# Performance work log

Measured on AMD Instinct MI355X. Metric: run time of the kernel, lower is better.

Reference implementation:

```python
import jax, jax.numpy as jnp
import numpy as np

NX, NY = 512, 512
NT = 240
STRIDE = 4
H = 1e-3
DT = 5e-8
F0 = 100000.0
T0 = 6e-6
AMP = 1.0
GAUSS_A = 5e6
RHO = 1600.0
C_INIT = dict(C11=1e11, C22=1e10, C12=8e9, C16=2.5e10, C26=3e9, C66=1.2e10)
C_LO, C_HI = 1e9, 1e13


def setup_inputs() -> dict:
    # Ricker wavelet source signal (full time resolution)
    t = np.arange(NT) * DT
    tau = t - T0
    pf = (np.pi * F0 * tau) ** 2
    signal = (AMP * (1.0 - 2.0 * pf) * np.exp(-pf)).astype(np.float32)
    # Gaussian point-load spatial distribution centered at (0,0)
    Lx, Ly = H * (NX - 1), H * (NY - 1)
    x = np.linspace(-Lx / 2, Lx / 2, NX, dtype=np.float64)
    y = np.linspace(-Ly / 2, Ly / 2, NY, dtype=np.float64)
    X, Y = np.meshgrid(x, y, indexing='ij')
    r2 = X ** 2 + Y ** 2
    gauss = (GAUSS_A / np.pi * np.exp(-GAUSS_A * r2)).astype(np.float32)
    return {
        'log_C11': jnp.array([np.log(C_INIT['C11'])], dtype=jnp.float32),
        'log_C22': jnp.array([np.log(C_INIT['C22'])], dtype=jnp.float32),
        'log_C12': jnp.array([np.log(C_INIT['C12'])], dtype=jnp.float32),
        'log_C16': jnp.array([np.log(C_INIT['C16'])], dtype=jnp.float32),
        'log_C26': jnp.array([np.log(C_INIT['C26'])], dtype=jnp.float32),
        'log_C66': jnp.array([np.log(C_INIT['C66'])], dtype=jnp.float32),
        'rho': jnp.array([RHO], dtype=jnp.float32),
        'source_signal': jnp.asarray(signal),
        'gaussian_dist': jnp.asarray(gauss),
    }


def _stencils(u, h_inv_sq):
    # u: (B, nx, ny), zero-padded 3x3 FD stencils (conv2d_fixed equivalent)
    p = jnp.pad(u, ((0, 0), (1, 1), (1, 1)))
    dxx = (p[:, 2:, 1:-1] + p[:, :-2, 1:-1] - 2.0 * u) * h_inv_sq
    dyy = (p[:, 1:-1, 2:] + p[:, 1:-1, :-2] - 2.0 * u) * h_inv_sq
    dxy = 0.25 * (p[:, :-2, :-2] - p[:, :-2, 2:] - p[:, 2:, :-2] + p[:, 2:, 2:]) * h_inv_sq
    return dxx, dyy, dxy


def _simulate(log_Cs, rho, source_signal, gaussian_dist):
    log_C11, log_C22, log_C12, log_C16, log_C26, log_C66 = log_Cs
    C11 = jnp.clip(jnp.exp(log_C11[0]), C_LO, C_HI)
    C22 = jnp.clip(jnp.exp(log_C22[0]), C_LO, C_HI)
    C12 = jnp.clip(jnp.exp(log_C12[0]), C_LO, C_HI)
    C16 = jnp.clip(jnp.exp(log_C16[0]), C_LO, C_HI)
    C26 = jnp.clip(jnp.exp(log_C26[0]), C_LO, C_HI)
    C66 = jnp.clip(jnp.exp(log_C66[0]), C_LO, C_HI)
    r = rho[0]
    h_inv_sq = jnp.float32(1.0 / (H * H))
    dt2 = jnp.float32(DT * DT)
    g = gaussian_dist[None]  # (1, nx, ny)
    zeros = jnp.zeros((1, NX, NY), dtype=jnp.float32)

    def step(carry, f_amp):
        ux1, uy1, ux2, uy2 = carry
        # source on y component
        force_y = f_amp * g
        dxx_ux, dyy_ux, dxy_ux = _stencils(ux1, h_inv_sq)
        dxx_uy, dyy_uy, dxy_uy = _stencils(uy1, h_inv_sq)
        Lux = (C11 * dxx_ux + C66 * dyy_ux + (C12 + C66) * dxy_uy
               + 2.0 * C16 * dxy_ux + C16 * dxx_uy + C26 * dyy_uy) / r
        Luy = (C66 * dxx_uy + C22 * dyy_uy + (C12 + C66) * dxy_ux
               + C16 * dxx_ux + C26 * dyy_ux + 2.0 * C26 * dxy_uy + force_y) / r
        ux_new = 2.0 * ux1 - ux2 + dt2 * Lux
        uy_new = 2.0 * uy1 - uy2 + dt2 * Luy
        return (ux_new, uy_new, ux1, uy1), (ux_new, uy_new)

    init = (zeros, zeros, zeros, zeros)
    _, (ux_hist, uy_hist) = jax.lax.scan(step, init, source_signal)
    # (nt, 1, nx, ny) -> (1, nt, nx, ny), then PRIMARY time stride subsample
    ux_fields = jnp.moveaxis(ux_hist, 0, 1)[:, ::STRIDE]
    uy_fields = jnp.moveaxis(uy_hist, 0, 1)[:, ::STRIDE]
    return ux_fields, uy_fields


def reference(log_C11, log_C22, log_C12, log_C16, log_C26, log_C66, rho, source_signal, gaussian_dist):
    return _simulate((log_C11, log_C22, log_C12, log_C16, log_C26, log_C66),
                     rho, source_signal, gaussian_dist)
```

## Files before the change

kernel.cpp:

```cpp
#include <hip/hip_runtime.h>

#define NXg    512
#define Sg     262144
#define NFRg   60
#define Kg     8
#define NCHUNK 30
#define TIg    32
#define TJg    16
#define EIg    48
#define EJg    32
#define RCIg   46
#define RCJg   30
#define CELg   (RCIg*RCJg)
#define NTHRg  512
#define NSLOTg 3

__global__ __launch_bounds__(NTHRg)
void cfrp_init(float* __restrict__ ws)
{
    const int gt = (int)blockIdx.x * NTHRg + (int)threadIdx.x;
    ((float4*)ws)[gt] = make_float4(0.f, 0.f, 0.f, 0.f);
}

__global__ __launch_bounds__(NTHRg, 4)
void cfrp_chunk(const float* __restrict__ lc11, const float* __restrict__ lc22,
                const float* __restrict__ lc12, const float* __restrict__ lc16,
                const float* __restrict__ lc26, const float* __restrict__ lc66,
                const float* __restrict__ rho_p, const float* __restrict__ sig,
                const float* __restrict__ gauss, float* __restrict__ out,
                const float* __restrict__ gcx, const float* __restrict__ gcy,
                const float* __restrict__ gpx, const float* __restrict__ gpy,
                float* __restrict__ ncx, float* __restrict__ ncy,
                float* __restrict__ npx, float* __restrict__ npy,
                int T0)
{
    __shared__ float sf[2][EIg * EJg * 2];

    const int tid = (int)threadIdx.x;
    const int bi = (int)blockIdx.x >> 5;
    const int bj = (int)blockIdx.x & 31;
    const int oi = bi * TIg - Kg;
    const int oj = bj * TJg - Kg;

    const float C11 = fminf(fmaxf(expf(lc11[0]), 1e9f), 1e13f);
    const float C22 = fminf(fmaxf(expf(lc22[0]), 1e9f), 1e13f);
    const float C12 = fminf(fmaxf(expf(lc12[0]), 1e9f), 1e13f);
    const float C16 = fminf(fmaxf(expf(lc16[0]), 1e9f), 1e13f);
    const float C26 = fminf(fmaxf(expf(lc26[0]), 1e9f), 1e13f);
    const float C66 = fminf(fmaxf(expf(lc66[0]), 1e9f), 1e13f);
    const float r    = rho_p[0];
    const float dt2  = 2.5e-15f;
    const float kk   = dt2 * 1e6f / r;
    const float kc11 = kk * C11, kc22 = kk * C22, kc66 = kk * C66;
    const float kc16 = kk * C16, kc26 = kk * C26;
    const float kc1266 = kk * (C12 + C66);
    const float kc16x2 = 2.0f * kc16;
    const float kc26x2 = 2.0f * kc26;
    const float gsc = dt2 / r;

    #pragma unroll
    for (int s = 0; s < NSLOTg; ++s) {
        const int idx = tid + s * NTHRg;
        const int rr = idx >> 5;
        const int cc = idx & 31;
        const int gi = oi + rr, gj = oj + cc;
        const bool inbb = ((unsigned)gi < NXg) && ((unsigned)gj < NXg);
        const int go = gi * NXg + gj;
        const float vx = inbb ? gcx[go] : 0.0f;
        const float vy = inbb ? gcy[go] : 0.0f;
        sf[0][2 * idx]     = vx;  sf[0][2 * idx + 1] = vy;
        sf[1][2 * idx]     = vx;  sf[1][2 * idx + 1] = vy;
    }

    int   la[NSLOTg], go[NSLOTg];
    float pvx[NSLOTg], pvy[NSLOTg], cvx[NSLOTg], cvy[NSLOTg], gfv[NSLOTg];
    bool  act[NSLOTg], inb[NSLOTg], own[NSLOTg];
    #pragma unroll
    for (int s = 0; s < NSLOTg; ++s) {
        const int idx = tid + s * NTHRg;
        act[s] = idx < CELg;
        const int ii = act[s] ? idx : 0;
        const int rr = ii / RCJg + 1;
        const int cc = ii - (rr - 1) * RCJg + 1;
        la[s] = ((rr << 5) + cc) * 2;
        const int gi = oi + rr, gj = oj + cc;
        inb[s] = ((unsigned)gi < NXg) && ((unsigned)gj < NXg);
        go[s] = gi * NXg + gj;
        own[s] = act[s] && rr >= Kg && rr < Kg + TIg
                        && cc >= Kg && cc < Kg + TJg;
        const bool ld = act[s] && inb[s];
        pvx[s] = ld ? gpx[go[s]] : 0.0f;
        pvy[s] = ld ? gpy[go[s]] : 0.0f;
        gfv[s] = ld ? gauss[go[s]] * gsc : 0.0f;
    }
    __syncthreads();

    #pragma unroll
    for (int s = 0; s < NSLOTg; ++s) {
        cvx[s] = sf[0][la[s]];
        cvy[s] = sf[0][la[s] + 1];
    }

    const float* cur = sf[0];
    float*       nxt = sf[1];

    #pragma unroll
    for (int st = 0; st < Kg; ++st) {
        const float fa = sig[T0 + st];
        #pragma unroll
        for (int s = 0; s < NSLOTg; ++s) {
            const int a = la[s];
            const float2 Nn = *(const float2*)&cur[a - 2 * EJg];
            const float2 Ss = *(const float2*)&cur[a + 2 * EJg];
            const float2 Ww = *(const float2*)&cur[a - 2];
            const float2 Ee = *(const float2*)&cur[a + 2];
            const float2 NW = *(const float2*)&cur[a - 2 * EJg - 2];
            const float2 NE = *(const float2*)&cur[a - 2 * EJg + 2];
            const float2 SW = *(const float2*)&cur[a + 2 * EJg - 2];
            const float2 SE = *(const float2*)&cur[a + 2 * EJg + 2];
            const float cx = cvx[s], cy = cvy[s];

            const float sxx_x = Nn.x + Ss.x - 2.0f * cx;
            const float syy_x = Ww.x + Ee.x - 2.0f * cx;
            const float sxy_x = 0.25f * (NW.x - NE.x - SW.x + SE.x);
            const float sxx_y = Nn.y + Ss.y - 2.0f * cy;
            const float syy_y = Ww.y + Ee.y - 2.0f * cy;
            const float sxy_y = 0.25f * (NW.y - NE.y - SW.y + SE.y);

            const float lux = kc11 * sxx_x + kc66 * syy_x + kc1266 * sxy_y
                            + kc16x2 * sxy_x + kc16 * sxx_y + kc26 * syy_y;
            const float luy = kc66 * sxx_y + kc22 * syy_y + kc1266 * sxy_x
                            + kc16 * sxx_x + kc26 * syy_x + kc26x2 * sxy_y
                            + fa * gfv[s];

            float vx = 2.0f * cx - pvx[s] + lux;
            float vy = 2.0f * cy - pvy[s] + luy;
            vx = inb[s] ? vx : 0.0f;
            vy = inb[s] ? vy : 0.0f;
            pvx[s] = cx;  pvy[s] = cy;
            cvx[s] = vx;  cvy[s] = vy;

            if (act[s]) {
                nxt[a]     = vx;
                nxt[a + 1] = vy;
            }
            if ((st & 3) == 0) {
                if (own[s]) {
                    const int fo = ((T0 + st) >> 2) * Sg + go[s];
                    out[fo] = vx;
                    out[fo + NFRg * Sg] = vy;
                }
            }
        }
        __syncthreads();
        float* tmp = (float*)cur; cur = nxt; nxt = tmp;
    }

    #pragma unroll
    for (int s = 0; s < NSLOTg; ++s) {
        if (own[s]) {
            ncx[go[s]] = cvx[s];
            ncy[go[s]] = cvy[s];
            npx[go[s]] = pvx[s];
            npy[go[s]] = pvy[s];
        }
    }
}

extern "C" void kernel_launch(void* const* d_in, const int* in_sizes, int n_in,
                              void* d_out, int out_size, void* d_ws, size_t ws_size,
                              hipStream_t stream) {
    const float* lc11  = (const float*)d_in[0];
    const float* lc22  = (const float*)d_in[1];
    const float* lc12  = (const float*)d_in[2];
    const float* lc16  = (const float*)d_in[3];
    const float* lc26  = (const float*)d_in[4];
    const float* lc66  = (const float*)d_in[5];
    const float* rho_p = (const float*)d_in[6];
    const float* sig   = (const float*)d_in[7];
    const float* gauss = (const float*)d_in[8];
    float* out = (float*)d_out;
    float* ws  = (float*)d_ws;

    float* A[4] = { ws,          ws + Sg,     ws + 2 * Sg, ws + 3 * Sg };
    float* B[4] = { ws + 4 * Sg, ws + 5 * Sg, ws + 6 * Sg, ws + 7 * Sg };

    hipLaunchKernelGGL(cfrp_init, dim3(Sg / NTHRg), dim3(NTHRg), 0, stream, ws);

    for (int c = 0; c < NCHUNK; ++c) {
        float** R = (c & 1) ? B : A;
        float** W = (c & 1) ? A : B;
        hipLaunchKernelGGL(cfrp_chunk, dim3(512), dim3(NTHRg), 0, stream,
                           lc11, lc22, lc12, lc16, lc26, lc66, rho_p, sig,
                           gauss, out,
                           R[0], R[1], R[2], R[3],
                           W[0], W[1], W[2], W[3],
                           c * Kg);
    }
}
```

Baseline: 674.3 us.

## Switch to 16x16 tiles with one cell per thread and interleaved float2 state

Each chunk block now covers a 16x16 owned tile with an 8-cell halo (30x30 computed region) using 1024 threads, one cell per thread, instead of 32x16 tiles with three cells per thread. The x/y displacement state is stored interleaved as float2 in global memory, which halves the number of state buffers. Blocks are remapped in a swizzled order, presumably for better cache locality. The aim is more parallelism and simpler per-thread code. In exchange, the halo-to-owned ratio rises, so more redundant stencil work is done, and about 124 threads per block sit idle.

```diff
diff --git a/kernel.cpp b/kernel.cpp
--- a/kernel.cpp
+++ b/kernel.cpp
@@ -5,42 +5,39 @@
 #define NFRg   60
 #define Kg     8
 #define NCHUNK 30
-#define TIg    32
-#define TJg    16
-#define EIg    48
-#define EJg    32
-#define RCIg   46
-#define RCJg   30
-#define CELg   (RCIg*RCJg)
-#define NTHRg  512
-#define NSLOTg 3
+#define Tg     16
+#define Eg     32
+#define RCg    30
+#define CELg   900
+#define NTB    1024
 
-__global__ __launch_bounds__(NTHRg)
-void cfrp_init(float* __restrict__ ws)
+__global__ __launch_bounds__(512)
+void cfrp_init(float2* __restrict__ ws2)
 {
-    const int gt = (int)blockIdx.x * NTHRg + (int)threadIdx.x;
-    ((float4*)ws)[gt] = make_float4(0.f, 0.f, 0.f, 0.f);
+    const int gt = (int)blockIdx.x * 512 + (int)threadIdx.x;
+    ws2[gt] = make_float2(0.f, 0.f);
 }
 
-__global__ __launch_bounds__(NTHRg, 4)
+__global__ __launch_bounds__(NTB, 8)
 void cfrp_chunk(const float* __restrict__ lc11, const float* __restrict__ lc22,
                 const float* __restrict__ lc12, const float* __restrict__ lc16,
                 const float* __restrict__ lc26, const float* __restrict__ lc66,
                 const float* __restrict__ rho_p, const float* __restrict__ sig,
                 const float* __restrict__ gauss, float* __restrict__ out,
-                const float* __restrict__ gcx, const float* __restrict__ gcy,
-                const float* __restrict__ gpx, const float* __restrict__ gpy,
-                float* __restrict__ ncx, float* __restrict__ ncy,
-                float* __restrict__ npx, float* __restrict__ npy,
+                const float2* __restrict__ gcur, const float2* __restrict__ gprev,
+                float2* __restrict__ ncur, float2* __restrict__ nprev,
                 int T0)
 {
-    __shared__ float sf[2][EIg * EJg * 2];
+    __shared__ float2 sf[2][Eg * Eg];
 
     const int tid = (int)threadIdx.x;
-    const int bi = (int)blockIdx.x >> 5;
-    const int bj = (int)blockIdx.x & 31;
-    const int oi = bi * TIg - Kg;
-    const int oj = bj * TJg - Kg;
+    const int w  = (int)blockIdx.x;
+    const int q  = w & 7;
+    const int r_ = w >> 3;
+    const int ti = q * 4 + (r_ >> 5);
+    const int tj = r_ & 31;
+    const int oi = ti * Tg - Kg;
+    const int oj = tj * Tg - Kg;
 
     const float C11 = fminf(fmaxf(expf(lc11[0]), 1e9f), 1e13f);
     const float C22 = fminf(fmaxf(expf(lc22[0]), 1e9f), 1e13f);
@@ -58,112 +55,88 @@
     const float kc26x2 = 2.0f * kc26;
     const float gsc = dt2 / r;
 
-    #pragma unroll
-    for (int s = 0; s < NSLOTg; ++s) {
-        const int idx = tid + s * NTHRg;
-        const int rr = idx >> 5;
-        const int cc = idx & 31;
+    {
+        const int rr = tid >> 5, cc = tid & 31;
         const int gi = oi + rr, gj = oj + cc;
         const bool inbb = ((unsigned)gi < NXg) && ((unsigned)gj < NXg);
-        const int go = gi * NXg + gj;
-        const float vx = inbb ? gcx[go] : 0.0f;
-        const float vy = inbb ? gcy[go] : 0.0f;
-        sf[0][2 * idx]     = vx;  sf[0][2 * idx + 1] = vy;
-        sf[1][2 * idx]     = vx;  sf[1][2 * idx + 1] = vy;
+        float2 v = make_float2(0.f, 0.f);
+        if (inbb) v = gcur[gi * NXg + gj];
+        sf[0][tid] = v;
+        sf[1][tid] = v;
     }
 
-    int   la[NSLOTg], go[NSLOTg];
-    float pvx[NSLOTg], pvy[NSLOTg], cvx[NSLOTg], cvy[NSLOTg], gfv[NSLOTg];
-    bool  act[NSLOTg], inb[NSLOTg], own[NSLOTg];
-    #pragma unroll
-    for (int s = 0; s < NSLOTg; ++s) {
-        const int idx = tid + s * NTHRg;
-        act[s] = idx < CELg;
-        const int ii = act[s] ? idx : 0;
-        const int rr = ii / RCJg + 1;
-        const int cc = ii - (rr - 1) * RCJg + 1;
-        la[s] = ((rr << 5) + cc) * 2;
-        const int gi = oi + rr, gj = oj + cc;
-        inb[s] = ((unsigned)gi < NXg) && ((unsigned)gj < NXg);
-        go[s] = gi * NXg + gj;
-        own[s] = act[s] && rr >= Kg && rr < Kg + TIg
-                        && cc >= Kg && cc < Kg + TJg;
-        const bool ld = act[s] && inb[s];
-        pvx[s] = ld ? gpx[go[s]] : 0.0f;
-        pvy[s] = ld ? gpy[go[s]] : 0.0f;
-        gfv[s] = ld ? gauss[go[s]] * gsc : 0.0f;
+    const bool activ = tid < CELg;
+    const int  ii = activ ? tid : (CELg - 1);
+    const int  rr = ii / RCg + 1;
+    const int  cc = ii - (rr - 1) * RCg + 1;
+    const int  la = (rr << 5) + cc;
+    const int  gi = oi + rr, gj = oj + cc;
+    const bool inb = ((unsigned)gi < NXg) && ((unsigned)gj < NXg);
+    const int  go = gi * NXg + gj;
+    const bool own = activ && rr >= Kg && rr < Kg + Tg
+                           && cc >= Kg && cc < Kg + Tg;
+    float2 pv = make_float2(0.f, 0.f);
+    float  gf = 0.f;
+    if (inb) {
+        pv = gprev[go];
+        gf = gauss[go] * gsc;
     }
     __syncthreads();
 
-    #pragma unroll
-    for (int s = 0; s < NSLOTg; ++s) {
-        cvx[s] = sf[0][la[s]];
-        cvy[s] = sf[0][la[s] + 1];
-    }
+    float2 cv = sf[0][la];
 
-    const float* cur = sf[0];
-    float*       nxt = sf[1];
+    const float2* cur = sf[0];
+    float2*       nxt = sf[1];
 
     #pragma unroll
     for (int st = 0; st < Kg; ++st) {
         const float fa = sig[T0 + st];
-        #pragma unroll
-        for (int s = 0; s < NSLOTg; ++s) {
-            const int a = la[s];
-            const float2 Nn = *(const float2*)&cur[a - 2 * EJg];
-            const float2 Ss = *(const float2*)&cur[a + 2 * EJg];
-            const float2 Ww = *(const float2*)&cur[a - 2];
-            const float2 Ee = *(const float2*)&cur[a + 2];
-            const float2 NW = *(const float2*)&cur[a - 2 * EJg - 2];
-            const float2 NE = *(const float2*)&cur[a - 2 * EJg + 2];
-            const float2 SW = *(const float2*)&cur[a + 2 * EJg - 2];
-            const float2 SE = *(const float2*)&cur[a + 2 * EJg + 2];
-            const float cx = cvx[s], cy = cvy[s];
+        const float2 Nn = cur[la - Eg];
+        const float2 Ss = cur[la + Eg];
+        const float2 Ww = cur[la - 1];
+        const float2 Ee = cur[la + 1];
+        const float2 NW = cur[la - Eg - 1];
+        const float2 NE = cur[la - Eg + 1];
+        const float2 SW = cur[la + Eg - 1];
+        const float2 SE = cur[la + Eg + 1];
+        const float cx = cv.x, cy = cv.y;
 
-            const float sxx_x = Nn.x + Ss.x - 2.0f * cx;
-            const float syy_x = Ww.x + Ee.x - 2.0f * cx;
-            const float sxy_x = 0.25f * (NW.x - NE.x - SW.x + SE.x);
-            const float sxx_y = Nn.y + Ss.y - 2.0f * cy;
-            const float syy_y = Ww.y + Ee.y - 2.0f * cy;
-            const float sxy_y = 0.25f * (NW.y - NE.y - SW.y + SE.y);
+        const float sxx_x = Nn.x + Ss.x - 2.0f * cx;
+        const float syy_x = Ww.x + Ee.x - 2.0f * cx;
+        const float sxy_x = 0.25f * (NW.x - NE.x - SW.x + SE.x);
+        const float sxx_y = Nn.y + Ss.y - 2.0f * cy;
+        const float syy_y = Ww.y + Ee.y - 2.0f * cy;
+        const float sxy_y = 0.25f * (NW.y - NE.y - SW.y + SE.y);
 
-            const float lux = kc11 * sxx_x + kc66 * syy_x + kc1266 * sxy_y
-                            + kc16x2 * sxy_x + kc16 * sxx_y + kc26 * syy_y;
-            const float luy = kc66 * sxx_y + kc22 * syy_y + kc1266 * sxy_x
-                            + kc16 * sxx_x + kc26 * syy_x + kc26x2 * sxy_y
-                            + fa * gfv[s];
+        const float lux = kc11 * sxx_x + kc66 * syy_x + kc1266 * sxy_y
+                        + kc16x2 * sxy_x + kc16 * sxx_y + kc26 * syy_y;
+        const float luy = kc66 * sxx_y + kc22 * syy_y + kc1266 * sxy_x
+                        + kc16 * sxx_x + kc26 * syy_x + kc26x2 * sxy_y
+                        + fa * gf;
 
-            float vx = 2.0f * cx - pvx[s] + lux;
-            float vy = 2.0f * cy - pvy[s] + luy;
-            vx = inb[s] ? vx : 0.0f;
-            vy = inb[s] ? vy : 0.0f;
-            pvx[s] = cx;  pvy[s] = cy;
-            cvx[s] = vx;  cvy[s] = vy;
+        float vx = 2.0f * cx - pv.x + lux;
+        float vy = 2.0f * cy - pv.y + luy;
+        vx = inb ? vx : 0.0f;
+        vy = inb ? vy : 0.0f;
+        pv = cv;
+        cv = make_float2(vx, vy);
 
-            if (act[s]) {
-                nxt[a]     = vx;
-                nxt[a + 1] = vy;
-            }
-            if ((st & 3) == 0) {
-                if (own[s]) {
-                    const int fo = ((T0 + st) >> 2) * Sg + go[s];
-                    out[fo] = vx;
-                    out[fo + NFRg * Sg] = vy;
-                }
+        nxt[la] = cv;
+
+        if ((st & 3) == 0) {
+            if (own) {
+                const int fo = ((T0 + st) >> 2) * Sg + go;
+                out[fo] = vx;
+                out[fo + NFRg * Sg] = vy;
             }
         }
         __syncthreads();
-        float* tmp = (float*)cur; cur = nxt; nxt = tmp;
+        float2* tmp = (float2*)cur; cur = nxt; nxt = tmp;
     }
 
-    #pragma unroll
-    for (int s = 0; s < NSLOTg; ++s) {
-        if (own[s]) {
-            ncx[go[s]] = cvx[s];
-            ncy[go[s]] = cvy[s];
-            npx[go[s]] = pvx[s];
-            npy[go[s]] = pvy[s];
-        }
+    if (own) {
+        ncur[go]  = cv;
+        nprev[go] = pv;
     }
 }
 
@@ -180,21 +153,19 @@
     const float* sig   = (const float*)d_in[7];
     const float* gauss = (const float*)d_in[8];
     float* out = (float*)d_out;
-    float* ws  = (float*)d_ws;
+    float2* ws2 = (float2*)d_ws;
 
-    float* A[4] = { ws,          ws + Sg,     ws + 2 * Sg, ws + 3 * Sg };
-    float* B[4] = { ws + 4 * Sg, ws + 5 * Sg, ws + 6 * Sg, ws + 7 * Sg };
+    float2* Ac = ws2;           float2* Ap = ws2 + Sg;
+    float2* Bc = ws2 + 2 * Sg;  float2* Bp = ws2 + 3 * Sg;
 
-    hipLaunchKernelGGL(cfrp_init, dim3(Sg / NTHRg), dim3(NTHRg), 0, stream, ws);
+    hipLaunchKernelGGL(cfrp_init, dim3(2 * Sg / 512), dim3(512), 0, stream, ws2);
 
     for (int c = 0; c < NCHUNK; ++c) {
-        float** R = (c & 1) ? B : A;
-        float** W = (c & 1) ? A : B;
-        hipLaunchKernelGGL(cfrp_chunk, dim3(512), dim3(NTHRg), 0, stream,
+        float2 *rc, *rp, *wc, *wp;
+        if (c & 1) { rc = Bc; rp = Bp; wc = Ac; wp = Ap; }
+        else       { rc = Ac; rp = Ap; wc = Bc; wp = Bp; }
+        hipLaunchKernelGGL(cfrp_chunk, dim3(1024), dim3(NTB), 0, stream,
                            lc11, lc22, lc12, lc16, lc26, lc66, rho_p, sig,
-                           gauss, out,
-                           R[0], R[1], R[2], R[3],
-                           W[0], W[1], W[2], W[3],
-                           c * Kg);
+                           gauss, out, rc, rp, wc, wp, c * Kg);
     }
 }
```

Result: no change. 663.8 us (-1.6%).
